# Optimization experiments

Hardware: AMD Instinct MI355X
Metric: run time of the kernel (lower is better)

## Reference

```python
import jax, jax.numpy as jnp
import numpy as np

DN = ('NHWC', 'HWIO', 'NHWC')

def _conv1x1(x, k):
    # 1x1 conv, stride 1, SAME padding (channels_last)
    return jax.lax.conv_general_dilated(x, k, window_strides=(1, 1), padding='SAME', dimension_numbers=DN)

def setup_inputs() -> dict:
    key = jax.random.key(0)
    k1, k2, k3, k4, k5 = jax.random.split(key, 5)
    B, H, W, C = 4, 64, 64, 256
    c8 = C // 8
    x = jax.random.normal(k1, (B, H, W, C), dtype=jnp.float32)
    # Glorot-like scaling for stability
    kernel_f = jax.random.normal(k2, (1, 1, C, c8), dtype=jnp.float32) * (1.0 / np.sqrt(C))
    kernel_g = jax.random.normal(k3, (1, 1, C, c8), dtype=jnp.float32) * (1.0 / np.sqrt(C))
    kernel_h = jax.random.normal(k4, (1, 1, C, C), dtype=jnp.float32) * (1.0 / np.sqrt(C))
    gamma = jax.random.normal(k5, (), dtype=jnp.float32) * 0.1
    return {'x': x, 'kernel_f': kernel_f, 'kernel_g': kernel_g, 'kernel_h': kernel_h, 'gamma': gamma}

def reference(x, kernel_f, kernel_g, kernel_h, gamma):
    B, H, W, C = x.shape
    N = H * W
    f = _conv1x1(x, kernel_f).reshape(B, N, -1)   # [B, N, C/8] queries
    g = _conv1x1(x, kernel_g).reshape(B, N, -1)   # [B, N, C/8] keys
    h = _conv1x1(x, kernel_h).reshape(B, N, -1)   # [B, N, C]   values
    e = jnp.einsum('bnc,bmc->bnm', f, g)          # [B, N, N] scores
    attn = jax.nn.softmax(e, axis=-1)
    o = jnp.einsum('bnm,bmc->bnc', attn, h).reshape(B, H, W, C)
    return x + gamma * o
```

## Files before the change

### kernel.cpp

```cpp
#include <hip/hip_runtime.h>

typedef __attribute__((ext_vector_type(8))) short bf16x8;
typedef __attribute__((ext_vector_type(4))) float f32x4;
typedef __attribute__((ext_vector_type(16))) float f32x16;

__device__ __forceinline__ unsigned short f2bf(float f) {
    union { float f; unsigned u; } v; v.f = f;
    return (unsigned short)((v.u + 0x7FFFu + ((v.u >> 16) & 1u)) >> 16);
}
__device__ __forceinline__ unsigned f2bf2_fast(float a, float b) {
    union { float f; unsigned u; } va, vb; va.f = a; vb.f = b;
    return ((va.u + 0x8000u) >> 16) | ((vb.u + 0x8000u) & 0xFFFF0000u);
}

__device__ __forceinline__ void async16(unsigned short* lds, const unsigned short* gsrc) {
    __builtin_amdgcn_global_load_lds(
        (const __attribute__((address_space(1))) void*)gsrc,
        (__attribute__((address_space(3))) void*)lds, 16, 0, 0);
}

__global__ __launch_bounds__(256) void k_wt(const float* __restrict__ kf,
                                            const float* __restrict__ kg,
                                            const float* __restrict__ kh,
                                            unsigned short* __restrict__ wt) {
    int n = blockIdx.x, t = threadIdx.x;
    const float* src; int stride, col;
    if (n < 32)      { src = kf; stride = 32;  col = n; }
    else if (n < 64) { src = kg; stride = 32;  col = n - 32; }
    else             { src = kh; stride = 256; col = n - 64; }
    wt[n * 256 + (((t >> 3) ^ (n & 7)) << 3) + (t & 7)] = f2bf(src[t * stride + col]);
}

__global__ __launch_bounds__(512) void k_proj(const float* __restrict__ x,
                                              const unsigned short* __restrict__ wt,
                                              unsigned short* __restrict__ f,
                                              unsigned short* __restrict__ g,
                                              unsigned short* __restrict__ hT) {
    __shared__ unsigned short xs[16384];
    __shared__ unsigned short ws[2][16384];
    int t = threadIdx.x, rb = blockIdx.x;
    int w = t >> 6, lane = t & 63, q = lane >> 4, n15 = lane & 15;
    int b = rb >> 6, nbase = (rb & 63) * 64;

#pragma unroll
    for (int i = 0; i < 8; ++i) {
        int lin = i * 512 + t, row = lin >> 6, c4 = lin & 63;
        float4 v = *(const float4*)&x[(rb * 64 + row) * 256 + c4 * 4];
        ushort4 o; o.x = f2bf(v.x); o.y = f2bf(v.y); o.z = f2bf(v.z); o.w = f2bf(v.w);
        *(ushort4*)&xs[row * 256 + (((c4 >> 1) ^ (row & 7)) << 3) + ((c4 & 1) << 2)] = o;
    }
#pragma unroll
    for (int j = 0; j < 4; ++j)
        async16(&ws[0][(j * 512 + w * 64) * 8], wt + (j * 512 + t) * 8);

    for (int ct = 0; ct < 5; ++ct) {
        int cur = ct & 1, nxt = cur ^ 1;
        __syncthreads();
        if (ct < 4) {
            const unsigned short* wsrc = wt + (ct + 1) * 16384;
#pragma unroll
            for (int j = 0; j < 4; ++j)
                async16(&ws[nxt][(j * 512 + w * 64) * 8], wsrc + (j * 512 + t) * 8);
        }
        const unsigned short* wcur = ws[cur];
        f32x4 acc[2];
        acc[0] = (f32x4){0.f, 0.f, 0.f, 0.f};
        acc[1] = (f32x4){0.f, 0.f, 0.f, 0.f};

        if (ct == 0) {
            int rg = w & 3, cg = w >> 2;
#pragma unroll
            for (int kk = 0; kk < 8; ++kk) {
                bf16x8 a = *(const bf16x8*)&xs[(rg * 16 + n15) * 256
                                + ((((kk << 2) + q) ^ (n15 & 7)) << 3)];
#pragma unroll
                for (int nt = 0; nt < 2; ++nt) {
                    bf16x8 bw = *(const bf16x8*)&wcur[(cg * 32 + nt * 16 + n15) * 256
                                    + ((((kk << 2) + q) ^ (n15 & 7)) << 3)];
                    acc[nt] = __builtin_amdgcn_mfma_f32_16x16x32_bf16(a, bw, acc[nt], 0, 0, 0);
                }
            }
#pragma unroll
            for (int nt = 0; nt < 2; ++nt)
#pragma unroll
                for (int r = 0; r < 4; ++r) {
                    int grow = rb * 64 + rg * 16 + q * 4 + r;
                    int col = cg * 32 + nt * 16 + n15;
                    unsigned short v = f2bf(acc[nt][r]);
                    if (col < 32) f[grow * 32 + col] = v;
                    else          g[grow * 32 + (col - 32)] = v;
                }
        } else {
            int cg = w & 3, rg = w >> 2;
#pragma unroll
            for (int kk = 0; kk < 8; ++kk) {
                bf16x8 a = *(const bf16x8*)&wcur[(cg * 16 + n15) * 256
                                + ((((kk << 2) + q) ^ (n15 & 7)) << 3)];
#pragma unroll
                for (int nt = 0; nt < 2; ++nt) {
                    bf16x8 bx = *(const bf16x8*)&xs[(rg * 32 + nt * 16 + n15) * 256
                                    + ((((kk << 2) + q) ^ (n15 & 7)) << 3)];
                    acc[nt] = __builtin_amdgcn_mfma_f32_16x16x32_bf16(a, bx, acc[nt], 0, 0, 0);
                }
            }
#pragma unroll
            for (int nt = 0; nt < 2; ++nt)
#pragma unroll
                for (int r = 0; r < 4; ++r) {
                    int ch = (ct - 1) * 64 + cg * 16 + q * 4 + r;
                    int nloc = nbase + rg * 32 + nt * 16 + n15;
                    hT[b * 1048576 + ch * 4096 + nloc] = f2bf(acc[nt][r]);
                }
        }
    }
}

__global__ __launch_bounds__(512, 4) void k_attn(const float* __restrict__ x,
                                                 const unsigned short* __restrict__ f,
                                                 const unsigned short* __restrict__ g,
                                                 const unsigned short* __restrict__ hT,
                                                 const float* __restrict__ gamma_p,
                                                 float* __restrict__ out) {
    __shared__ unsigned short hs[2][8192];
    __shared__ unsigned short pls[2][4096];
    __shared__ float lrec[64];
    int t = threadIdx.x, bx = blockIdx.x;
    int b = (bx >> 1) & 3;
    int ch2 = (bx >> 3) & 1;
    int qt = ((bx & 1) << 5) | (bx >> 4);
    int qbase = qt * 64;
    int chbase = ch2 * 128;
    int w = t >> 6, l = t & 63;
    int hi = l >> 5, l31 = l & 31;
    int q = l >> 4, n15 = l & 15;
    int cb = w & 3;
    const bool is_s = (w < 4);

    bf16x8 aFB;
    if (is_s)
        aFB = *(const bf16x8*)&f[(b * 4096 + qbase + w * 16 + n15) * 32 + q * 8];

    const unsigned short* hsrc = hT + b * 1048576 + (chbase + (t >> 3)) * 4096
                               + (((t & 7) ^ ((t >> 3) & 7)) << 3);

    const unsigned short* gbase = g + (b * 4096 + n15) * 32 + q * 8;
    bf16x8 aG[4], aGn[4];

    f32x16 o0, o1;
#pragma unroll
    for (int i = 0; i < 16; ++i) { o0[i] = 0.f; o1[i] = 0.f; }
    float l_acc = 0.f;
    const f32x4 zero4 = (f32x4){0.f, 0.f, 0.f, 0.f};

    auto s_tile = [&](int buf) {
        f32x4 sa[4];
#pragma unroll
        for (int nt = 0; nt < 4; ++nt)
            sa[nt] = __builtin_amdgcn_mfma_f32_16x16x32_bf16(aG[nt], aFB, zero4, 0, 0, 0);
#pragma unroll
        for (int nt = 0; nt < 4; ++nt)
#pragma unroll
            for (int r = 0; r < 4; ++r) {
                sa[nt][r] = __expf(sa[nt][r]);
                l_acc += sa[nt][r];
            }
#pragma unroll
        for (int nt = 0; nt < 4; ++nt) {
            unsigned p0 = f2bf2_fast(sa[nt][0], sa[nt][1]);
            unsigned p1 = f2bf2_fast(sa[nt][2], sa[nt][3]);
            int kq = 4 * nt + q;
            unsigned* dst = (unsigned*)&pls[buf][(w * 16 + n15) * 64]
                          + ((kq >> 1) ^ (n15 & 7)) * 4 + (kq & 1) * 2;
            dst[0] = p0; dst[1] = p1;
        }
    };

    async16(&hs[0][w * 512], hsrc);
    async16(&hs[0][4096 + w * 512], hsrc + 64 * 4096);
    if (is_s) {
#pragma unroll
        for (int nt = 0; nt < 4; ++nt)
            aG[nt] = *(const bf16x8*)&gbase[(nt * 16) * 32];
#pragma unroll
        for (int nt = 0; nt < 4; ++nt)
            aGn[nt] = *(const bf16x8*)&gbase[(64 + nt * 16) * 32];
        s_tile(0);
#pragma unroll
        for (int nt = 0; nt < 4; ++nt) aG[nt] = aGn[nt];
    }
    __syncthreads();

    for (int kt = 0; kt < 64; ++kt) {
        int cur = kt & 1, nxt = cur ^ 1;

        if (kt + 1 < 64) {
            const unsigned short* hp = hsrc + (kt + 1) * 64;
            async16(&hs[nxt][w * 512], hp);
            async16(&hs[nxt][4096 + w * 512], hp + 64 * 4096);
        }

        if (is_s) {
            if (kt + 1 < 64) {
                int ktn = (kt + 2 < 64) ? kt + 2 : 63;
#pragma unroll
                for (int nt = 0; nt < 4; ++nt)
                    aGn[nt] = *(const bf16x8*)&gbase[(ktn * 64 + nt * 16) * 32];
                s_tile(nxt);
#pragma unroll
                for (int nt = 0; nt < 4; ++nt) aG[nt] = aGn[nt];
            }
        } else {
            const unsigned short* hcur = &hs[cur][0];
            const unsigned short* pcur = &pls[cur][0];
#pragma unroll
            for (int ks = 0; ks < 4; ++ks) {
                int seg = (((2 * ks + hi) ^ (l31 & 7)) << 3);
                bf16x8 bH  = *(const bf16x8*)&hcur[(cb * 32 + l31) * 64 + seg];
                bf16x8 aP0 = *(const bf16x8*)&pcur[l31 * 64 + seg];
                bf16x8 aP1 = *(const bf16x8*)&pcur[(32 + l31) * 64 + seg];
                o0 = __builtin_amdgcn_mfma_f32_32x32x16_bf16(aP0, bH, o0, 0, 0, 0);
                o1 = __builtin_amdgcn_mfma_f32_32x32x16_bf16(aP1, bH, o1, 0, 0, 0);
            }
        }

        __syncthreads();
    }

    if (is_s) {
        float ps = l_acc;
        ps += __shfl_xor(ps, 16);
        ps += __shfl_xor(ps, 32);
        if (q == 0) lrec[w * 16 + n15] = 1.0f / ps;
    }
    __syncthreads();
    if (!is_s) {
        float gam = *gamma_p;
        int ch = chbase + cb * 32 + l31;
#pragma unroll
        for (int qq = 0; qq < 4; ++qq) {
            int r0 = 8 * qq + 4 * hi;
            f32x4 ri0 = *(const f32x4*)&lrec[r0];
            f32x4 ri1 = *(const f32x4*)&lrec[32 + r0];
#pragma unroll
            for (int j = 0; j < 4; ++j) {
                int idx0 = (b * 4096 + qbase + r0 + j) * 256 + ch;
                int idx1 = idx0 + 32 * 256;
                out[idx0] = x[idx0] + gam * (o0[4 * qq + j] * ri0[j]);
                out[idx1] = x[idx1] + gam * (o1[4 * qq + j] * ri1[j]);
            }
        }
    }
}

extern "C" void kernel_launch(void* const* d_in, const int* in_sizes, int n_in,
                              void* d_out, int out_size, void* d_ws, size_t ws_size,
                              hipStream_t stream) {
    const float* x  = (const float*)d_in[0];
    const float* kf = (const float*)d_in[1];
    const float* kg = (const float*)d_in[2];
    const float* kh = (const float*)d_in[3];
    const float* gm = (const float*)d_in[4];
    float* out = (float*)d_out;

    char* ws = (char*)d_ws;
    unsigned short* wt = (unsigned short*)(ws);
    unsigned short* fb = (unsigned short*)(ws + 163840);
    unsigned short* gb = (unsigned short*)(ws + 1212416);
    unsigned short* hT = (unsigned short*)(ws + 2260992);

    hipLaunchKernelGGL(k_wt,   dim3(320), dim3(256), 0, stream, kf, kg, kh, wt);
    hipLaunchKernelGGL(k_proj, dim3(256), dim3(512), 0, stream, x, wt, fb, gb, hT);
    hipLaunchKernelGGL(k_attn, dim3(512), dim3(512), 0, stream, x, fb, gb, hT, gm, out);
}
```

Before: 151.3 us.

## Split PV waves into 2x2 register tiles with K-split and LDS merge

The four PV waves previously each owned 32 channels across 64 rows, reloading both P fragments per channel block. Now each wave computes a 64x64 output tile (2x2 MFMA 32x32 blocks) over half of the K dimension, so every P and H fragment read from LDS feeds two MFMAs. The two K-halves are summed through an LDS merge at the end. A new XOR swizzle key (mixing row bits) replaces the simple row&7 swizzle to avoid bank conflicts with the new access pattern. Accumulator registers double to 64 floats per lane, which may pressure occupancy, and there is an extra LDS reduction step.

```diff
diff --git a/kernel.cpp b/kernel.cpp
--- a/kernel.cpp
+++ b/kernel.cpp
@@ -3,6 +3,8 @@
 typedef __attribute__((ext_vector_type(8))) short bf16x8;
 typedef __attribute__((ext_vector_type(4))) float f32x4;
 typedef __attribute__((ext_vector_type(16))) float f32x16;
+
+#define KEY(r) ((((r) & 7) ^ (3 * ((r) >> 3))) & 7)
 
 __device__ __forceinline__ unsigned short f2bf(float f) {
     union { float f; unsigned u; } v; v.f = f;
@@ -133,24 +135,43 @@
     int w = t >> 6, l = t & 63;
     int hi = l >> 5, l31 = l & 31;
     int q = l >> 4, n15 = l & 15;
-    int cb = w & 3;
     const bool is_s = (w < 4);
+    int cb = (w >> 1) & 1, kh = w & 1;
 
     bf16x8 aFB;
-    if (is_s)
+    int pkey = 0;
+    if (is_s) {
         aFB = *(const bf16x8*)&f[(b * 4096 + qbase + w * 16 + n15) * 32 + q * 8];
-
-    const unsigned short* hsrc = hT + b * 1048576 + (chbase + (t >> 3)) * 4096
-                               + (((t & 7) ^ ((t >> 3) & 7)) << 3);
+        pkey = KEY(w * 16 + n15);
+    }
+
+    int chL0 = t >> 3, chL1 = 64 + (t >> 3);
+    const unsigned short* hsrc0 = hT + b * 1048576 + (chbase + chL0) * 4096
+                                + (((t & 7) ^ KEY(chL0)) << 3);
+    const unsigned short* hsrc1 = hT + b * 1048576 + (chbase + chL1) * 4096
+                                + (((t & 7) ^ KEY(chL1)) << 3);
 
     const unsigned short* gbase = g + (b * 4096 + n15) * 32 + q * 8;
     bf16x8 aG[4], aGn[4];
 
-    f32x16 o0, o1;
-#pragma unroll
-    for (int i = 0; i < 16; ++i) { o0[i] = 0.f; o1[i] = 0.f; }
+    f32x16 oo[4];
+#pragma unroll
+    for (int a = 0; a < 4; ++a)
+#pragma unroll
+        for (int i = 0; i < 16; ++i) oo[a][i] = 0.f;
     float l_acc = 0.f;
     const f32x4 zero4 = (f32x4){0.f, 0.f, 0.f, 0.f};
+
+    int sA0a = 0, sA0b = 0, sA1a = 0, sA1b = 0;
+    int sH0a = 0, sH0b = 0, sH1a = 0, sH1b = 0, rH0 = 0, rH1 = 0;
+    if (!is_s) {
+        int e0 = 4 * kh + hi, e1 = e0 + 2;
+        sA0a = (e0 ^ KEY(l31)) << 3;       sA0b = (e1 ^ KEY(l31)) << 3;
+        sA1a = (e0 ^ KEY(32 + l31)) << 3;  sA1b = (e1 ^ KEY(32 + l31)) << 3;
+        rH0 = cb * 64 + l31; rH1 = rH0 + 32;
+        sH0a = (e0 ^ KEY(rH0)) << 3;       sH0b = (e1 ^ KEY(rH0)) << 3;
+        sH1a = (e0 ^ KEY(rH1)) << 3;       sH1b = (e1 ^ KEY(rH1)) << 3;
+    }
 
     auto s_tile = [&](int buf) {
         f32x4 sa[4];
@@ -170,13 +191,13 @@
             unsigned p1 = f2bf2_fast(sa[nt][2], sa[nt][3]);
             int kq = 4 * nt + q;
             unsigned* dst = (unsigned*)&pls[buf][(w * 16 + n15) * 64]
-                          + ((kq >> 1) ^ (n15 & 7)) * 4 + (kq & 1) * 2;
+                          + ((kq >> 1) ^ pkey) * 4 + (kq & 1) * 2;
             dst[0] = p0; dst[1] = p1;
         }
     };
 
-    async16(&hs[0][w * 512], hsrc);
-    async16(&hs[0][4096 + w * 512], hsrc + 64 * 4096);
+    async16(&hs[0][w * 512], hsrc0);
+    async16(&hs[0][4096 + w * 512], hsrc1);
     if (is_s) {
 #pragma unroll
         for (int nt = 0; nt < 4; ++nt)
@@ -194,9 +215,8 @@
         int cur = kt & 1, nxt = cur ^ 1;
 
         if (kt + 1 < 64) {
-            const unsigned short* hp = hsrc + (kt + 1) * 64;
-            async16(&hs[nxt][w * 512], hp);
-            async16(&hs[nxt][4096 + w * 512], hp + 64 * 4096);
+            async16(&hs[nxt][w * 512], hsrc0 + (kt + 1) * 64);
+            async16(&hs[nxt][4096 + w * 512], hsrc1 + (kt + 1) * 64);
         }
 
         if (is_s) {
@@ -212,15 +232,22 @@
         } else {
             const unsigned short* hcur = &hs[cur][0];
             const unsigned short* pcur = &pls[cur][0];
-#pragma unroll
-            for (int ks = 0; ks < 4; ++ks) {
-                int seg = (((2 * ks + hi) ^ (l31 & 7)) << 3);
-                bf16x8 bH  = *(const bf16x8*)&hcur[(cb * 32 + l31) * 64 + seg];
-                bf16x8 aP0 = *(const bf16x8*)&pcur[l31 * 64 + seg];
-                bf16x8 aP1 = *(const bf16x8*)&pcur[(32 + l31) * 64 + seg];
-                o0 = __builtin_amdgcn_mfma_f32_32x32x16_bf16(aP0, bH, o0, 0, 0, 0);
-                o1 = __builtin_amdgcn_mfma_f32_32x32x16_bf16(aP1, bH, o1, 0, 0, 0);
-            }
+            bf16x8 aP0 = *(const bf16x8*)&pcur[l31 * 64 + sA0a];
+            bf16x8 aP1 = *(const bf16x8*)&pcur[(32 + l31) * 64 + sA1a];
+            bf16x8 bH0 = *(const bf16x8*)&hcur[rH0 * 64 + sH0a];
+            bf16x8 bH1 = *(const bf16x8*)&hcur[rH1 * 64 + sH1a];
+            oo[0] = __builtin_amdgcn_mfma_f32_32x32x16_bf16(aP0, bH0, oo[0], 0, 0, 0);
+            oo[1] = __builtin_amdgcn_mfma_f32_32x32x16_bf16(aP0, bH1, oo[1], 0, 0, 0);
+            oo[2] = __builtin_amdgcn_mfma_f32_32x32x16_bf16(aP1, bH0, oo[2], 0, 0, 0);
+            oo[3] = __builtin_amdgcn_mfma_f32_32x32x16_bf16(aP1, bH1, oo[3], 0, 0, 0);
+            aP0 = *(const bf16x8*)&pcur[l31 * 64 + sA0b];
+            aP1 = *(const bf16x8*)&pcur[(32 + l31) * 64 + sA1b];
+            bH0 = *(const bf16x8*)&hcur[rH0 * 64 + sH0b];
+            bH1 = *(const bf16x8*)&hcur[rH1 * 64 + sH1b];
+            oo[0] = __builtin_amdgcn_mfma_f32_32x32x16_bf16(aP0, bH0, oo[0], 0, 0, 0);
+            oo[1] = __builtin_amdgcn_mfma_f32_32x32x16_bf16(aP0, bH1, oo[1], 0, 0, 0);
+            oo[2] = __builtin_amdgcn_mfma_f32_32x32x16_bf16(aP1, bH0, oo[2], 0, 0, 0);
+            oo[3] = __builtin_amdgcn_mfma_f32_32x32x16_bf16(aP1, bH1, oo[3], 0, 0, 0);
         }
 
         __syncthreads();
@@ -232,23 +259,40 @@
         ps += __shfl_xor(ps, 32);
         if (q == 0) lrec[w * 16 + n15] = 1.0f / ps;
     }
+    float* mrg = (float*)&hs[0][0];
+    if (!is_s && kh == 1) {
+        int base = (cb * 64 + l) * 64;
+#pragma unroll
+        for (int a = 0; a < 4; ++a)
+            *(f32x16*)&mrg[base + a * 16] = oo[a];
+    }
     __syncthreads();
-    if (!is_s) {
+    if (!is_s && kh == 0) {
+        int base = (cb * 64 + l) * 64;
+#pragma unroll
+        for (int a = 0; a < 4; ++a) {
+            f32x16 m = *(const f32x16*)&mrg[base + a * 16];
+#pragma unroll
+            for (int i = 0; i < 16; ++i) oo[a][i] += m[i];
+        }
         float gam = *gamma_p;
-        int ch = chbase + cb * 32 + l31;
-#pragma unroll
-        for (int qq = 0; qq < 4; ++qq) {
-            int r0 = 8 * qq + 4 * hi;
-            f32x4 ri0 = *(const f32x4*)&lrec[r0];
-            f32x4 ri1 = *(const f32x4*)&lrec[32 + r0];
-#pragma unroll
-            for (int j = 0; j < 4; ++j) {
-                int idx0 = (b * 4096 + qbase + r0 + j) * 256 + ch;
-                int idx1 = idx0 + 32 * 256;
-                out[idx0] = x[idx0] + gam * (o0[4 * qq + j] * ri0[j]);
-                out[idx1] = x[idx1] + gam * (o1[4 * qq + j] * ri1[j]);
-            }
-        }
+#pragma unroll
+        for (int rb2 = 0; rb2 < 2; ++rb2)
+#pragma unroll
+            for (int c2 = 0; c2 < 2; ++c2) {
+                int a = rb2 * 2 + c2;
+                int ch = chbase + cb * 64 + c2 * 32 + l31;
+#pragma unroll
+                for (int qq = 0; qq < 4; ++qq) {
+                    int r0 = rb2 * 32 + 8 * qq + 4 * hi;
+                    f32x4 ri = *(const f32x4*)&lrec[r0];
+#pragma unroll
+                    for (int j = 0; j < 4; ++j) {
+                        int idx = (b * 4096 + qbase + r0 + j) * 256 + ch;
+                        out[idx] = x[idx] + gam * (oo[a][4 * qq + j] * ri[j]);
+                    }
+                }
+            }
     }
 }
 
```

Measured after the change: 160.4 us. +6.0%, slower.
